# Optimization experiments

Hardware: AMD Instinct MI355X
Metric: run time of the kernel (lower is better)

## Reference

```python
import jax, jax.numpy as jnp
import numpy as np

B, S, H = 1, 2048, 4096
NH, NKV, HD = 32, 8, 128
MAX_POS, ROPE_THETA = 4096, 10000.0


def setup_inputs() -> dict:
    key = jax.random.key(0)
    ks = jax.random.split(key, 6)
    hidden_states = jax.random.normal(ks[0], (B, S, H), dtype=jnp.float32)
    # additive causal mask (0 on/below diagonal, large negative above)
    causal = jnp.tril(jnp.ones((S, S), dtype=bool))
    attention_mask = jnp.where(causal, 0.0, -1e9).astype(jnp.float32)[None, None]
    position_ids = jnp.broadcast_to(jnp.arange(S, dtype=jnp.int32)[None, :], (B, S))
    sc = 0.02
    Wq = jax.random.normal(ks[1], (H, NH * HD), dtype=jnp.float32) * sc
    Wk = jax.random.normal(ks[2], (H, NKV * HD), dtype=jnp.float32) * sc
    Wv = jax.random.normal(ks[3], (H, NKV * HD), dtype=jnp.float32) * sc
    Wo = jax.random.normal(ks[4], (NH * HD, H), dtype=jnp.float32) * sc
    return {"hidden_states": hidden_states, "attention_mask": attention_mask,
            "position_ids": position_ids, "Wq": Wq, "Wk": Wk, "Wv": Wv, "Wo": Wo}


def _rotate_half(x):
    x1, x2 = x[..., : x.shape[-1] // 2], x[..., x.shape[-1] // 2 :]
    return jnp.concatenate((-x2, x1), axis=-1)


def _rope_tables(seq_len, dtype):
    inv_freq = 1.0 / (ROPE_THETA ** (jnp.arange(0, HD, 2, dtype=jnp.float32) / HD))
    t = jnp.arange(seq_len, dtype=jnp.float32)
    freqs = jnp.einsum("i,j->ij", t, inv_freq)        # [S, HD/2]
    emb = jnp.concatenate((freqs, freqs), axis=-1)     # [S, HD]
    return jnp.cos(emb).astype(dtype), jnp.sin(emb).astype(dtype)


def reference(hidden_states, attention_mask, position_ids, Wq, Wk, Wv, Wo):
    bsz, q_len, _ = hidden_states.shape
    # projections -> [b, h, s, d]
    q = (hidden_states @ Wq).reshape(bsz, q_len, NH, HD).swapaxes(1, 2)
    k = (hidden_states @ Wk).reshape(bsz, q_len, NKV, HD).swapaxes(1, 2)
    v = (hidden_states @ Wv).reshape(bsz, q_len, NKV, HD).swapaxes(1, 2)
    # rotary embedding
    cos, sin = _rope_tables(q_len, hidden_states.dtype)
    cos = jnp.take(cos, position_ids, axis=0)[:, None]  # [b,1,s,d]
    sin = jnp.take(sin, position_ids, axis=0)[:, None]
    q = q * cos + _rotate_half(q) * sin
    k = k * cos + _rotate_half(k) * sin
    # GQA: repeat kv heads
    n_rep = NH // NKV
    k = jnp.repeat(k, n_rep, axis=1)
    v = jnp.repeat(v, n_rep, axis=1)
    # attention
    scores = jnp.einsum("bhqd,bhkd->bhqk", q, k) / jnp.sqrt(jnp.float32(HD)).astype(q.dtype)
    scores = scores + attention_mask
    attn = jax.nn.softmax(scores, axis=-1)
    out = jnp.einsum("bhqk,bhkd->bhqd", attn, v)
    out = out.swapaxes(1, 2).reshape(bsz, q_len, NH * HD)
    return out @ Wo
```

## Files before the change

kernel.cpp:

```cpp
#include <hip/hip_runtime.h>

typedef unsigned short u16;
typedef __attribute__((ext_vector_type(8))) __bf16 bf16x8;
typedef __attribute__((ext_vector_type(4))) __bf16 bf16x4;
typedef __attribute__((ext_vector_type(8))) unsigned short u16x8;
typedef __attribute__((ext_vector_type(4))) unsigned short u16x4;
typedef __attribute__((ext_vector_type(4))) float f32x4;

#define AS1 __attribute__((address_space(1)))
#define AS3 __attribute__((address_space(3)))

__device__ __forceinline__ void load_lds16(const void* g, void* l) {
  __builtin_amdgcn_global_load_lds((const AS1 unsigned int*)g,
                                   (AS3 unsigned int*)l, 16, 0, 0);
}

__device__ __forceinline__ float bf2f(u16 u) {
  unsigned int x = ((unsigned int)u) << 16;
  return __builtin_bit_cast(float, x);
}
__device__ __forceinline__ u16 f2bf(float f) {
  unsigned int x = __builtin_bit_cast(unsigned int, f);
  x += 0x7fffu + ((x >> 16) & 1u);
  return (u16)(x >> 16);
}
__device__ __forceinline__ bf16x8 cvt8(const float* p) {
  f32x4 a = *(const f32x4*)p;
  f32x4 b = *(const f32x4*)(p + 4);
  u16x8 r;
#pragma unroll
  for (int j = 0; j < 4; ++j) { r[j] = f2bf(a[j]); r[4 + j] = f2bf(b[j]); }
  return __builtin_bit_cast(bf16x8, r);
}

__global__ __launch_bounds__(256) void cvt_bf16_kernel(const float* __restrict__ in,
                                                       u16* __restrict__ out) {
  const int i = (blockIdx.x * 256 + threadIdx.x) * 8;
  *(bf16x8*)&out[i] = cvt8(in + i);
}

__global__ __launch_bounds__(256) void transpose_w(const float* __restrict__ in,
                                                   u16* __restrict__ out,
                                                   int R, int C, int col0) {
  __shared__ u16 tile[32][33];
  const int tx = threadIdx.x & 31, ty = threadIdx.x >> 5;
  const int c0 = blockIdx.x * 32, r0 = blockIdx.y * 32;
#pragma unroll
  for (int j = ty; j < 32; j += 8)
    tile[j][tx] = f2bf(in[(size_t)(r0 + j) * C + col0 + c0 + tx]);
  __syncthreads();
#pragma unroll
  for (int j = ty; j < 32; j += 8)
    out[(size_t)(c0 + j) * R + r0 + tx] = tile[tx][j];
}

__device__ __forceinline__ void stage_tile2(const u16* Ag, const u16* Bg,
                                            u16* Asb, u16* Bsb, int w, int K,
                                            int k0) {
#pragma unroll
  for (int j = 0; j < 2; ++j)
    load_lds16(Ag + (size_t)j * 64 * K + k0, Asb + j * 4096 + w * 512);
#pragma unroll
  for (int j = 0; j < 4; ++j)
    load_lds16(Bg + (size_t)j * 64 * K + k0, Bsb + j * 4096 + w * 512);
}

template <int MODE>
__global__ __launch_bounds__(512, 2) void gemm2(const u16* __restrict__ A,
                                                const u16* __restrict__ Bt,
                                                void* __restrict__ Cv,
                                                u16* __restrict__ C2,
                                                int K, int ldC) {
  __shared__ __align__(16) u16 As[3][128 * 64];
  __shared__ __align__(16) u16 Bs[3][256 * 64];
  const int tid = threadIdx.x, lane = tid & 63, w = tid >> 6;
  const int quad = lane >> 4, c16 = lane & 15;
  const int bm = blockIdx.x * 128, bn = blockIdx.y * 256;
  const int wm = (w >> 2) * 64, wn = (w & 3) * 64;

  const int l3 = lane >> 3, l7 = lane & 7;
  const int ss = l7 ^ l3;
  const u16* Ag = A + (size_t)(bm + w * 8 + l3) * K + ss * 8;
  const u16* Bg = Bt + (size_t)(bn + w * 8 + l3) * K + ss * 8;
  const int sx = (c16 & 7) << 4;

  f32x4 acc[4][4] = {};
  const int NT = K >> 6;

  stage_tile2(Ag, Bg, As[0], Bs[0], w, K, 0);
  stage_tile2(Ag, Bg, As[1], Bs[1], w, K, 64);
  int bc = 0;
  for (int kt = 0; kt < NT; ++kt) {
    if (kt < NT - 1)
      asm volatile("s_waitcnt vmcnt(6)" ::: "memory");
    else
      asm volatile("s_waitcnt vmcnt(0)" ::: "memory");
    __builtin_amdgcn_s_barrier();
    asm volatile("" ::: "memory");
    const int bp = bc + 2 >= 3 ? bc - 1 : bc + 2;
    if (kt + 2 < NT) stage_tile2(Ag, Bg, As[bp], Bs[bp], w, K, (kt + 2) << 6);

    const u16* Ab = As[bc];
    const u16* Bb = Bs[bc];
    bf16x8 a[4][2], b[4][2];
#pragma unroll
    for (int mt = 0; mt < 4; ++mt)
#pragma unroll
      for (int kc = 0; kc < 2; ++kc) {
        const int row = wm + mt * 16 + c16;
        a[mt][kc] = *(const bf16x8*)&Ab[(row * 128 + ((((kc * 4 + quad) << 4)) ^ sx)) >> 1];
      }
#pragma unroll
    for (int nt = 0; nt < 4; ++nt)
#pragma unroll
      for (int kc = 0; kc < 2; ++kc) {
        const int row = wn + nt * 16 + c16;
        b[nt][kc] = *(const bf16x8*)&Bb[(row * 128 + ((((kc * 4 + quad) << 4)) ^ sx)) >> 1];
      }
    __builtin_amdgcn_s_setprio(1);
#pragma unroll
    for (int kc = 0; kc < 2; ++kc)
#pragma unroll
      for (int mt = 0; mt < 4; ++mt)
#pragma unroll
        for (int nt = 0; nt < 4; ++nt)
          acc[mt][nt] = __builtin_amdgcn_mfma_f32_16x16x32_bf16(a[mt][kc], b[nt][kc], acc[mt][nt], 0, 0, 0);
    __builtin_amdgcn_s_setprio(0);
    bc = bc == 2 ? 0 : bc + 1;
  }
#pragma unroll
  for (int mt = 0; mt < 4; ++mt)
#pragma unroll
    for (int nt = 0; nt < 4; ++nt)
#pragma unroll
      for (int r = 0; r < 4; ++r) {
        const int row = bm + wm + mt * 16 + quad * 4 + r;
        const int col = bn + wn + nt * 16 + c16;
        if (MODE == 1)
          ((float*)Cv)[(size_t)row * ldC + col] = acc[mt][nt][r];
        else if (MODE == 0)
          ((u16*)Cv)[(size_t)row * ldC + col] = f2bf(acc[mt][nt][r]);
        else {
          if (bn < 1024)
            ((u16*)Cv)[(size_t)row * 1024 + col] = f2bf(acc[mt][nt][r]);
          else
            C2[(size_t)(col - 1024) * 2048 + row] = f2bf(acc[mt][nt][r]);
        }
      }
}

__global__ void rope_kernel(u16* __restrict__ buf, const int* __restrict__ pos,
                            int log2nh, float oscale) {
  const int t = blockIdx.x * 256 + threadIdx.x;
  const int i = t & 63;
  const int h = (t >> 6) & ((1 << log2nh) - 1);
  const int s = t >> (6 + log2nh);
  const int nh = 1 << log2nh;
  const float p = (float)pos[s];
  const float invf = exp2f((float)i * -0.20762051915861040f);
  const float ang = p * invf;
  const float cn = cosf(ang), sn = sinf(ang);
  const size_t i1 = (size_t)s * (nh * 128) + h * 128 + i;
  const size_t i2 = i1 + 64;
  const float x1 = bf2f(buf[i1]), x2 = bf2f(buf[i2]);
  buf[i1] = f2bf((x1 * cn - x2 * sn) * oscale);
  buf[i2] = f2bf((x2 * cn + x1 * sn) * oscale);
}

__global__ __launch_bounds__(256, 2) void flash_kernel(const u16* __restrict__ Q,
                                                       const u16* __restrict__ K,
                                                       const u16* __restrict__ VT,
                                                       u16* __restrict__ O) {
  __shared__ __align__(16) u16 Ks[64 * 128];
  __shared__ __align__(16) u16 Vts[128 * 64];
  __shared__ __align__(16) u16 Ps[4][16 * 68];
  const int h = blockIdx.x, kvh = h >> 2;
  const int qb = 31 - blockIdx.y;
  const int tid = threadIdx.x, lane = tid & 63, w = tid >> 6;
  const int quad = lane >> 4, c16 = lane & 15;
  const int rw = lane >> 2, c4 = lane & 3;
  const int sw = (rw & 7) << 3;
  const int sr = (c16 & 7) << 3;

  bf16x8 aq[4];
#pragma unroll
  for (int kc = 0; kc < 4; ++kc)
    aq[kc] = *(const bf16x8*)&Q[(size_t)(qb * 64 + w * 16 + c16) * 4096 + h * 128 + kc * 32 + quad * 8];

  f32x4 acc_o[8] = {};
  float m_run[4], l_run[4];
#pragma unroll
  for (int r = 0; r < 4; ++r) { m_run[r] = -1e30f; l_run[r] = 0.f; }

  bf16x8 kc_[4], vc_[4];
#pragma unroll
  for (int p = 0; p < 4; ++p) {
    kc_[p] = *(const bf16x8*)&K[(size_t)(w * 16 + rw) * 1024 + kvh * 128 + p * 32 + c4 * 8];
    const int d = (p & 1) * 64 + w * 16 + rw;
    vc_[p] = *(const bf16x8*)&VT[(size_t)(kvh * 128 + d) * 2048 + (p >> 1) * 32 + c4 * 8];
  }

  for (int t = 0; t <= qb; ++t) {
    __syncthreads();
    const int key = w * 16 + rw;
#pragma unroll
    for (int p = 0; p < 4; ++p) {
      *(bf16x8*)&Ks[key * 128 + ((p * 32 + c4 * 8) ^ sw)] = kc_[p];
      const int d = (p & 1) * 64 + w * 16 + rw;
      *(bf16x8*)&Vts[d * 64 + ((((p >> 1) * 32 + c4 * 8)) ^ ((d & 7) << 3))] = vc_[p];
    }
    __syncthreads();
    if (t < qb) {
#pragma unroll
      for (int p = 0; p < 4; ++p) {
        kc_[p] = *(const bf16x8*)&K[(size_t)((t + 1) * 64 + w * 16 + rw) * 1024 + kvh * 128 + p * 32 + c4 * 8];
        const int d = (p & 1) * 64 + w * 16 + rw;
        vc_[p] = *(const bf16x8*)&VT[(size_t)(kvh * 128 + d) * 2048 + (t + 1) * 64 + (p >> 1) * 32 + c4 * 8];
      }
    }

    f32x4 sacc[4];
    __builtin_amdgcn_s_setprio(1);
#pragma unroll
    for (int nt = 0; nt < 4; ++nt) {
      f32x4 s = {0.f, 0.f, 0.f, 0.f};
#pragma unroll
      for (int kc = 0; kc < 4; ++kc) {
        bf16x8 bk = *(const bf16x8*)&Ks[(nt * 16 + c16) * 128 + ((kc * 32 + quad * 8) ^ sr)];
        s = __builtin_amdgcn_mfma_f32_16x16x32_bf16(aq[kc], bk, s, 0, 0, 0);
      }
      sacc[nt] = s;
    }
    __builtin_amdgcn_s_setprio(0);
    if (t == qb) {
#pragma unroll
      for (int nt = 0; nt < 4; ++nt)
#pragma unroll
        for (int r = 0; r < 4; ++r)
          if (nt * 16 + c16 > w * 16 + quad * 4 + r) sacc[nt][r] = -1e30f;
    }
    float al[4];
#pragma unroll
    for (int r = 0; r < 4; ++r) {
      float mx = fmaxf(fmaxf(sacc[0][r], sacc[1][r]), fmaxf(sacc[2][r], sacc[3][r]));
#pragma unroll
      for (int off = 1; off < 16; off <<= 1) mx = fmaxf(mx, __shfl_xor(mx, off));
      const float nm = fmaxf(m_run[r], mx);
      al[r] = __expf(m_run[r] - nm);
      m_run[r] = nm;
      float sum = 0.f;
#pragma unroll
      for (int nt = 0; nt < 4; ++nt) {
        const float pv = __expf(sacc[nt][r] - nm);
        sacc[nt][r] = pv;
        sum += pv;
      }
#pragma unroll
      for (int off = 1; off < 16; off <<= 1) sum += __shfl_xor(sum, off);
      l_run[r] = l_run[r] * al[r] + sum;
    }
#pragma unroll
    for (int dt = 0; dt < 8; ++dt)
#pragma unroll
      for (int r = 0; r < 4; ++r) acc_o[dt][r] *= al[r];
#pragma unroll
    for (int nt = 0; nt < 4; ++nt)
#pragma unroll
      for (int r = 0; r < 4; ++r)
        Ps[w][(quad * 4 + r) * 68 + nt * 16 + c16] = f2bf(sacc[nt][r]);
    asm volatile("s_waitcnt lgkmcnt(0)" ::: "memory");
    bf16x8 ap[2];
#pragma unroll
    for (int kc = 0; kc < 2; ++kc) {
      const u16* pp = &Ps[w][c16 * 68 + kc * 32 + quad * 8];
      bf16x4 lo = *(const bf16x4*)pp;
      bf16x4 hi = *(const bf16x4*)(pp + 4);
      bf16x8 apv;
#pragma unroll
      for (int j = 0; j < 4; ++j) { apv[j] = lo[j]; apv[4 + j] = hi[j]; }
      ap[kc] = apv;
    }
    __builtin_amdgcn_s_setprio(1);
#pragma unroll
    for (int dt = 0; dt < 8; ++dt)
#pragma unroll
      for (int kc = 0; kc < 2; ++kc) {
        bf16x8 bv = *(const bf16x8*)&Vts[(dt * 16 + c16) * 64 + ((kc * 32 + quad * 8) ^ sr)];
        acc_o[dt] = __builtin_amdgcn_mfma_f32_16x16x32_bf16(ap[kc], bv, acc_o[dt], 0, 0, 0);
      }
    __builtin_amdgcn_s_setprio(0);
  }
#pragma unroll
  for (int r = 0; r < 4; ++r) {
    const float inv = 1.0f / l_run[r];
    const int row = qb * 64 + w * 16 + quad * 4 + r;
#pragma unroll
    for (int dt = 0; dt < 8; ++dt)
      O[(size_t)row * 4096 + h * 128 + dt * 16 + c16] = f2bf(acc_o[dt][r] * inv);
  }
}

extern "C" void kernel_launch(void* const* d_in, const int* in_sizes, int n_in,
                              void* d_out, int out_size, void* d_ws, size_t ws_size,
                              hipStream_t stream) {
  const float* X  = (const float*)d_in[0];
  const int* pos  = (const int*)d_in[2];
  const float* Wq = (const float*)d_in[3];
  const float* Wk = (const float*)d_in[4];
  const float* Wv = (const float*)d_in[5];
  const float* Wo = (const float*)d_in[6];
  float* out = (float*)d_out;

  const int NP = (ws_size >= (size_t)50331648) ? 4096 : 2048;
  char* ws = (char*)d_ws;
  u16* WT  = (u16*)ws;
  u16* Att = (u16*)(ws + (NP == 4096 ? 33554432 : 16777216));
  u16* Xb  = Att;
  u16* Qb  = (u16*)d_out;
  u16* Kb  = (u16*)((char*)d_out + 16777216);
  u16* VTb = (u16*)((char*)d_out + 20971520);

  const dim3 b256(256), b512(512);

  cvt_bf16_kernel<<<dim3(4096), b256, 0, stream>>>(X, Xb);

  for (int p = 0; p < 4096; p += NP) {
    transpose_w<<<dim3(NP / 32, 128), b256, 0, stream>>>(Wq, WT, 4096, 4096, p);
    gemm2<0><<<dim3(16, NP / 256), b512, 0, stream>>>(Xb, WT, Qb + p, nullptr, 4096, 4096);
  }
  transpose_w<<<dim3(32, 128), b256, 0, stream>>>(Wk, WT, 4096, 1024, 0);
  transpose_w<<<dim3(32, 128), b256, 0, stream>>>(Wv, WT + (size_t)1024 * 4096, 4096, 1024, 0);
  gemm2<2><<<dim3(16, 8), b512, 0, stream>>>(Xb, WT, Kb, VTb, 4096, 0);

  rope_kernel<<<dim3(2048 * 32 * 64 / 256), b256, 0, stream>>>(Qb, pos, 5, 0.08838834764831845f);
  rope_kernel<<<dim3(2048 * 8 * 64 / 256),  b256, 0, stream>>>(Kb, pos, 3, 1.0f);

  flash_kernel<<<dim3(32, 32), b256, 0, stream>>>(Qb, Kb, VTb, Att);

  for (int p = 0; p < 4096; p += NP) {
    transpose_w<<<dim3(NP / 32, 128), b256, 0, stream>>>(Wo, WT, 4096, 4096, p);
    gemm2<1><<<dim3(16, NP / 256), b512, 0, stream>>>(Att, WT, out + p, nullptr, 4096, 4096);
  }
}
```

Before: 608.6 us.

## Remap GEMM block order and rework workspace layout for single-pass Q projection

Changes the gemm2 block-to-tile mapping so that consecutive workgroups share M rows and sweep N tiles, with a special interleaving for the 16-wide grid, aiming for better L2 reuse. It also reorganizes workspace and output buffer aliasing so the Q projection always runs as one full transpose plus GEMM launch, even with the small workspace. This removes a split launch pair. The aliasing of Xb, Qb, Kb and VTb into d_out and the workspace is more intricate and could overlap if the sizes are misjudged.

```diff
diff --git a/kernel.cpp b/kernel.cpp
--- a/kernel.cpp
+++ b/kernel.cpp
@@ -75,7 +75,12 @@
   __shared__ __align__(16) u16 Bs[3][256 * 64];
   const int tid = threadIdx.x, lane = tid & 63, w = tid >> 6;
   const int quad = lane >> 4, c16 = lane & 15;
-  const int bm = blockIdx.x * 128, bn = blockIdx.y * 256;
+
+  const int f = blockIdx.y * gridDim.x + blockIdx.x;
+  int bm, bn;
+  if (gridDim.y == 16) { bn = ((f & 7) * 2 + ((f >> 3) & 1)) * 256; bm = (f >> 4) * 128; }
+  else                 { bn = (f & 7) * 256;                        bm = (f >> 3) * 128; }
+
   const int wm = (w >> 2) * 64, wn = (w & 3) * 64;
 
   const int l3 = lane >> 3, l7 = lane & 7;
@@ -311,34 +316,48 @@
   const float* Wo = (const float*)d_in[6];
   float* out = (float*)d_out;
 
-  const int NP = (ws_size >= (size_t)50331648) ? 4096 : 2048;
+  const int big = ws_size >= (size_t)50331648;
   char* ws = (char*)d_ws;
-  u16* WT  = (u16*)ws;
-  u16* Att = (u16*)(ws + (NP == 4096 ? 33554432 : 16777216));
-  u16* Xb  = Att;
-  u16* Qb  = (u16*)d_out;
-  u16* Kb  = (u16*)((char*)d_out + 16777216);
-  u16* VTb = (u16*)((char*)d_out + 20971520);
+  u16* WTq  = (u16*)ws;
+  u16* WTkv = (u16*)ws;
+  u16* Att, *Xb, *Qb, *Kb, *VTb, *WTo;
+  int NPo;
+  if (big) {
+    Att = (u16*)(ws + 33554432);
+    Xb  = Att;
+    Qb  = (u16*)d_out;
+    Kb  = (u16*)((char*)d_out + 16777216);
+    VTb = (u16*)((char*)d_out + 20971520);
+    WTo = (u16*)ws;
+    NPo = 4096;
+  } else {
+    Att = (u16*)ws;
+    Xb  = (u16*)d_out;
+    Qb  = (u16*)((char*)d_out + 16777216);
+    Kb  = (u16*)(ws + 16777216);
+    VTb = (u16*)(ws + 20971520);
+    WTo = (u16*)(ws + 16777216);
+    NPo = 2048;
+  }
 
   const dim3 b256(256), b512(512);
 
   cvt_bf16_kernel<<<dim3(4096), b256, 0, stream>>>(X, Xb);
 
-  for (int p = 0; p < 4096; p += NP) {
-    transpose_w<<<dim3(NP / 32, 128), b256, 0, stream>>>(Wq, WT, 4096, 4096, p);
-    gemm2<0><<<dim3(16, NP / 256), b512, 0, stream>>>(Xb, WT, Qb + p, nullptr, 4096, 4096);
-  }
-  transpose_w<<<dim3(32, 128), b256, 0, stream>>>(Wk, WT, 4096, 1024, 0);
-  transpose_w<<<dim3(32, 128), b256, 0, stream>>>(Wv, WT + (size_t)1024 * 4096, 4096, 1024, 0);
-  gemm2<2><<<dim3(16, 8), b512, 0, stream>>>(Xb, WT, Kb, VTb, 4096, 0);
+  transpose_w<<<dim3(128, 128), b256, 0, stream>>>(Wq, WTq, 4096, 4096, 0);
+  gemm2<0><<<dim3(16, 16), b512, 0, stream>>>(Xb, WTq, Qb, nullptr, 4096, 4096);
+
+  transpose_w<<<dim3(32, 128), b256, 0, stream>>>(Wk, WTkv, 4096, 1024, 0);
+  transpose_w<<<dim3(32, 128), b256, 0, stream>>>(Wv, WTkv + (size_t)1024 * 4096, 4096, 1024, 0);
+  gemm2<2><<<dim3(16, 8), b512, 0, stream>>>(Xb, WTkv, Kb, VTb, 4096, 0);
 
   rope_kernel<<<dim3(2048 * 32 * 64 / 256), b256, 0, stream>>>(Qb, pos, 5, 0.08838834764831845f);
   rope_kernel<<<dim3(2048 * 8 * 64 / 256),  b256, 0, stream>>>(Kb, pos, 3, 1.0f);
 
   flash_kernel<<<dim3(32, 32), b256, 0, stream>>>(Qb, Kb, VTb, Att);
 
-  for (int p = 0; p < 4096; p += NP) {
-    transpose_w<<<dim3(NP / 32, 128), b256, 0, stream>>>(Wo, WT, 4096, 4096, p);
-    gemm2<1><<<dim3(16, NP / 256), b512, 0, stream>>>(Att, WT, out + p, nullptr, 4096, 4096);
-  }
-}
+  for (int p = 0; p < 4096; p += NPo) {
+    transpose_w<<<dim3(NPo / 32, 128), b256, 0, stream>>>(Wo, WTo, 4096, 4096, p);
+    gemm2<1><<<dim3(16, NPo / 256), b512, 0, stream>>>(Att, WTo, out + p, nullptr, 4096, 4096);
+  }
+}
```

After: 608.0 us. No clear change (-0.1%).
